# Optimization experiments

Hardware: AMD Instinct MI355X
Metric: run time of the kernel (lower is better)

Reference implementation:

```python
import jax, jax.numpy as jnp
import numpy as np

EPS = 1e-08
N_CODECS = 1024

def setup_inputs() -> dict:
    key = jax.random.key(0)
    indices = jax.random.randint(key, (16, 1048576), 0, N_CODECS, dtype=jnp.int64 if jax.config.jax_enable_x64 else jnp.int32)
    return {"indices": indices}

def reference(indices) -> jnp.ndarray:
    # Faithful to: encodings = eq(arange[:,None], flat[None,:]); probs = mean(encodings, dim=1)
    # mean of one-hot over N == count/N, so use a histogram (bincount) instead of the
    # O(n_codecs x N) boolean matrix.
    flat = indices.reshape(-1)
    counts = jnp.bincount(flat, length=N_CODECS)  # [n_codecs]
    probs = counts.astype(jnp.float32) / flat.shape[0]
    perplexity = jnp.exp(-jnp.sum(probs * jnp.log(probs + EPS)))
    return perplexity
```

## Files before the change

kernel.cpp:

```cpp
#include <hip/hip_runtime.h>

#define N_CODECS 1024
#define EPS 1e-8f
#define HIST_BLOCKS 1024
#define RED_BLOCKS 128
#define RED_THREADS 512
#define ROWS_PER_RED (HIST_BLOCKS / RED_BLOCKS)

__global__ void __launch_bounds__(256) hist_partial_kernel(
        const int* __restrict__ idx,
        unsigned int* __restrict__ gpart,
        unsigned int* __restrict__ cnt,
        unsigned int* __restrict__ done,
        int n4) {
    __shared__ unsigned int lcounts[N_CODECS];
    #pragma unroll
    for (int i = threadIdx.x; i < N_CODECS; i += 256) lcounts[i] = 0u;

    if (blockIdx.x == 0) {
        #pragma unroll
        for (int i = threadIdx.x; i < N_CODECS; i += 256) cnt[i] = 0u;
        if (threadIdx.x == 0) done[0] = 0u;
    }
    __syncthreads();

    const int4* __restrict__ idx4 = (const int4*)idx;
    const int stride = gridDim.x * 256;
    for (int i = blockIdx.x * 256 + threadIdx.x; i < n4; i += 2 * stride) {
        int4 a = idx4[i];
        int j = i + stride;
        bool has_b = (j < n4);
        int4 b = has_b ? idx4[j] : make_int4(0, 0, 0, 0);

        atomicAdd(&lcounts[a.x], 1u);
        atomicAdd(&lcounts[a.y], 1u);
        atomicAdd(&lcounts[a.z], 1u);
        atomicAdd(&lcounts[a.w], 1u);
        if (has_b) {
            atomicAdd(&lcounts[b.x], 1u);
            atomicAdd(&lcounts[b.y], 1u);
            atomicAdd(&lcounts[b.z], 1u);
            atomicAdd(&lcounts[b.w], 1u);
        }
    }
    __syncthreads();

    unsigned int* __restrict__ mypart = gpart + (size_t)blockIdx.x * N_CODECS;
    #pragma unroll
    for (int i = 0; i < N_CODECS / 256; ++i) {
        int b = i * 256 + threadIdx.x;
        mypart[b] = lcounts[b];
    }
}

__global__ void __launch_bounds__(RED_THREADS) reduce_finalize_kernel(
        const unsigned int* __restrict__ gpart,
        unsigned int* __restrict__ cnt,
        unsigned int* __restrict__ done,
        float* __restrict__ out,
        float invN) {
    int t = threadIdx.x;

    const unsigned int* __restrict__ base =
        gpart + (size_t)(blockIdx.x * ROWS_PER_RED) * N_CODECS;
    unsigned int s0 = 0, s1 = 0;
    #pragma unroll
    for (int r = 0; r < ROWS_PER_RED; ++r) {
        s0 += base[(size_t)r * N_CODECS + t];
        s1 += base[(size_t)r * N_CODECS + t + RED_THREADS];
    }
    atomicAdd(&cnt[t], s0);
    atomicAdd(&cnt[t + RED_THREADS], s1);

    __syncthreads();

    __shared__ unsigned int ticket;
    if (t == 0) {
        __threadfence();
        ticket = atomicAdd(done, 1u);
    }
    __syncthreads();
    if (ticket != (unsigned int)(RED_BLOCKS - 1)) return;

    __threadfence();
    unsigned int c0 = atomicAdd(&cnt[t], 0u);
    unsigned int c1 = atomicAdd(&cnt[t + RED_THREADS], 0u);
    float p0 = (float)c0 * invN;
    float p1 = (float)c1 * invN;
    float term = p0 * logf(p0 + EPS) + p1 * logf(p1 + EPS);

    #pragma unroll
    for (int off = 32; off > 0; off >>= 1) term += __shfl_down(term, off, 64);

    __shared__ float wsum[RED_THREADS / 64];
    int wave = t >> 6;
    int lane = t & 63;
    if (lane == 0) wsum[wave] = term;
    __syncthreads();

    if (t == 0) {
        float s = 0.0f;
        #pragma unroll
        for (int w = 0; w < RED_THREADS / 64; ++w) s += wsum[w];
        out[0] = expf(-s);
    }
}

extern "C" void kernel_launch(void* const* d_in, const int* in_sizes, int n_in,
                              void* d_out, int out_size, void* d_ws, size_t ws_size,
                              hipStream_t stream) {
    const int* indices = (const int*)d_in[0];
    int n = in_sizes[0];
    float* out = (float*)d_out;

    unsigned int* gpart = (unsigned int*)d_ws;
    unsigned int* cnt   = gpart + (size_t)HIST_BLOCKS * N_CODECS;
    unsigned int* done  = cnt + N_CODECS;

    int n4 = n >> 2;

    hist_partial_kernel<<<HIST_BLOCKS, 256, 0, stream>>>(indices, gpart, cnt, done, n4);
    reduce_finalize_kernel<<<RED_BLOCKS, RED_THREADS, 0, stream>>>(
        gpart, cnt, done, out, 1.0f / (float)n);
}
```

Measured before the change: 94.91 us.

## Replicate shared histogram 32 ways per bin to cut LDS atomic conflicts

Each block now keeps 32 copies of every histogram bin in LDS (128 KB), laid out so that lanes with different sub-indices land in different banks. This is meant to cut same-address contention and bank conflicts on the LDS atomics. Blocks become larger (1024 threads) and fewer (256), and each block folds its replicas into one partial row using a rotated read pattern. The reduce kernel switches to 1024 threads with one bin per thread. The cost is lower occupancy, since only one block fits per CU, plus extra time to zero and fold the larger shared array.

```diff
diff --git a/kernel.cpp b/kernel.cpp
--- a/kernel.cpp
+++ b/kernel.cpp
@@ -2,55 +2,63 @@
 
 #define N_CODECS 1024
 #define EPS 1e-8f
-#define HIST_BLOCKS 1024
-#define RED_BLOCKS 128
-#define RED_THREADS 512
+#define REP 32
+#define HIST_BLOCKS 256
+#define HIST_THREADS 1024
+#define RED_BLOCKS 64
+#define RED_THREADS 1024
 #define ROWS_PER_RED (HIST_BLOCKS / RED_BLOCKS)
 
-__global__ void __launch_bounds__(256) hist_partial_kernel(
+__global__ void __launch_bounds__(HIST_THREADS) hist_partial_kernel(
         const int* __restrict__ idx,
         unsigned int* __restrict__ gpart,
         unsigned int* __restrict__ cnt,
         unsigned int* __restrict__ done,
         int n4) {
-    __shared__ unsigned int lcounts[N_CODECS];
+    __shared__ unsigned int lc[N_CODECS * REP];
+
+    const int t = threadIdx.x;
+
+    uint4* lc4 = (uint4*)lc;
     #pragma unroll
-    for (int i = threadIdx.x; i < N_CODECS; i += 256) lcounts[i] = 0u;
+    for (int k = 0; k < (N_CODECS * REP / 4) / HIST_THREADS; ++k)
+        lc4[k * HIST_THREADS + t] = make_uint4(0u, 0u, 0u, 0u);
 
     if (blockIdx.x == 0) {
         #pragma unroll
-        for (int i = threadIdx.x; i < N_CODECS; i += 256) cnt[i] = 0u;
-        if (threadIdx.x == 0) done[0] = 0u;
+        for (int i = t; i < N_CODECS; i += HIST_THREADS) cnt[i] = 0u;
+        if (t == 0) done[0] = 0u;
     }
     __syncthreads();
 
     const int4* __restrict__ idx4 = (const int4*)idx;
-    const int stride = gridDim.x * 256;
-    for (int i = blockIdx.x * 256 + threadIdx.x; i < n4; i += 2 * stride) {
+    const int S = gridDim.x * HIST_THREADS;
+    const int sub = t & 31;
+    for (int i = blockIdx.x * HIST_THREADS + t; i < n4; i += 2 * S) {
         int4 a = idx4[i];
-        int j = i + stride;
+        int j = i + S;
         bool has_b = (j < n4);
         int4 b = has_b ? idx4[j] : make_int4(0, 0, 0, 0);
 
-        atomicAdd(&lcounts[a.x], 1u);
-        atomicAdd(&lcounts[a.y], 1u);
-        atomicAdd(&lcounts[a.z], 1u);
-        atomicAdd(&lcounts[a.w], 1u);
+        atomicAdd(&lc[(a.x << 5) | sub], 1u);
+        atomicAdd(&lc[(a.y << 5) | sub], 1u);
+        atomicAdd(&lc[(a.z << 5) | sub], 1u);
+        atomicAdd(&lc[(a.w << 5) | sub], 1u);
         if (has_b) {
-            atomicAdd(&lcounts[b.x], 1u);
-            atomicAdd(&lcounts[b.y], 1u);
-            atomicAdd(&lcounts[b.z], 1u);
-            atomicAdd(&lcounts[b.w], 1u);
+            atomicAdd(&lc[(b.x << 5) | sub], 1u);
+            atomicAdd(&lc[(b.y << 5) | sub], 1u);
+            atomicAdd(&lc[(b.z << 5) | sub], 1u);
+            atomicAdd(&lc[(b.w << 5) | sub], 1u);
         }
     }
     __syncthreads();
 
-    unsigned int* __restrict__ mypart = gpart + (size_t)blockIdx.x * N_CODECS;
+    unsigned int sum = 0;
+    const int base = t << 5;
     #pragma unroll
-    for (int i = 0; i < N_CODECS / 256; ++i) {
-        int b = i * 256 + threadIdx.x;
-        mypart[b] = lcounts[b];
-    }
+    for (int s = 0; s < REP; ++s)
+        sum += lc[base | ((s + t) & 31)];
+    gpart[(size_t)blockIdx.x * N_CODECS + t] = sum;
 }
 
 __global__ void __launch_bounds__(RED_THREADS) reduce_finalize_kernel(
@@ -63,14 +71,11 @@
 
     const unsigned int* __restrict__ base =
         gpart + (size_t)(blockIdx.x * ROWS_PER_RED) * N_CODECS;
-    unsigned int s0 = 0, s1 = 0;
+    unsigned int s0 = 0;
     #pragma unroll
-    for (int r = 0; r < ROWS_PER_RED; ++r) {
+    for (int r = 0; r < ROWS_PER_RED; ++r)
         s0 += base[(size_t)r * N_CODECS + t];
-        s1 += base[(size_t)r * N_CODECS + t + RED_THREADS];
-    }
     atomicAdd(&cnt[t], s0);
-    atomicAdd(&cnt[t + RED_THREADS], s1);
 
     __syncthreads();
 
@@ -83,11 +88,9 @@
     if (ticket != (unsigned int)(RED_BLOCKS - 1)) return;
 
     __threadfence();
-    unsigned int c0 = atomicAdd(&cnt[t], 0u);
-    unsigned int c1 = atomicAdd(&cnt[t + RED_THREADS], 0u);
-    float p0 = (float)c0 * invN;
-    float p1 = (float)c1 * invN;
-    float term = p0 * logf(p0 + EPS) + p1 * logf(p1 + EPS);
+    unsigned int c = atomicAdd(&cnt[t], 0u);
+    float p = (float)c * invN;
+    float term = p * logf(p + EPS);
 
     #pragma unroll
     for (int off = 32; off > 0; off >>= 1) term += __shfl_down(term, off, 64);
@@ -119,7 +122,8 @@
 
     int n4 = n >> 2;
 
-    hist_partial_kernel<<<HIST_BLOCKS, 256, 0, stream>>>(indices, gpart, cnt, done, n4);
+    hist_partial_kernel<<<HIST_BLOCKS, HIST_THREADS, 0, stream>>>(
+        indices, gpart, cnt, done, n4);
     reduce_finalize_kernel<<<RED_BLOCKS, RED_THREADS, 0, stream>>>(
         gpart, cnt, done, out, 1.0f / (float)n);
 }
```

After: 96.08 us. Within noise of the previous version (+1.2%).
